# Performance work log

Measured on AMD Instinct MI355X. Metric: run time of the kernel, lower is better.

Reference implementation:

```python
import jax, jax.numpy as jnp
import numpy as np

B, T, C, H = 2, 2048, 1024, 16


def setup_inputs() -> dict:
    key = jax.random.key(0)
    ks = jax.random.split(key, 9)
    s = 1.0 / np.sqrt(C)
    return {
        "query": jax.random.normal(ks[0], (B, T, C), dtype=jnp.float32),
        "Wq": jax.random.normal(ks[1], (C, C), dtype=jnp.float32) * s,
        "bq": jnp.zeros((C,), dtype=jnp.float32),
        "Wk": jax.random.normal(ks[2], (C, C), dtype=jnp.float32) * s,
        "bk": jnp.zeros((C,), dtype=jnp.float32),
        "Wv": jax.random.normal(ks[3], (C, C), dtype=jnp.float32) * s,
        "bv": jnp.zeros((C,), dtype=jnp.float32),
        "Wp": jax.random.normal(ks[4], (C, C), dtype=jnp.float32) * s,
        "bp": jnp.zeros((C,), dtype=jnp.float32),
        "n_head": H,
    }


def reference(query, Wq, bq, Wk, bk, Wv, bv, Wp, bp, n_head):
    b, t, c = query.shape
    d = c // n_head
    # QKV projections -> [b, h, t, d]
    q = (query @ Wq + bq).reshape(b, t, n_head, d).transpose(0, 2, 1, 3)
    k = (query @ Wk + bk).reshape(b, t, n_head, d).transpose(0, 2, 1, 3)
    v = (query @ Wv + bv).reshape(b, t, n_head, d).transpose(0, 2, 1, 3)
    scale = 1.0 / jnp.sqrt(jnp.asarray(d, dtype=query.dtype))
    att = jnp.einsum('bhtd,bhsd->bhts', q, k) * scale  # [b,h,t,t]
    causal = jnp.tril(jnp.ones((t, t), dtype=bool))
    att = jnp.where(causal[None, None, :, :], att, -jnp.inf)
    att = jax.nn.softmax(att, axis=-1)
    y = jnp.einsum('bhts,bhsd->bhtd', att, v)  # [b,h,t,d]
    y = y.transpose(0, 2, 1, 3).reshape(b, t, c)
    return y @ Wp + bp
```

## Files before the change

kernel.cpp:

```cpp
#include <hip/hip_runtime.h>
#include <math.h>

#define B_ 2
#define T_ 2048
#define C_ 1024
#define H_ 16
#define D_ 64
#define M_ (B_*T_)

typedef __bf16 bf16x8 __attribute__((ext_vector_type(8)));
typedef __bf16 bf16x4 __attribute__((ext_vector_type(4)));
typedef float  f32x4  __attribute__((ext_vector_type(4)));
typedef float  f32x16 __attribute__((ext_vector_type(16)));

__device__ __forceinline__ unsigned short f2bf(float f) {
    unsigned int u = __float_as_uint(f);
    u += 0x7FFFu + ((u >> 16) & 1u);
    return (unsigned short)(u >> 16);
}

__device__ __forceinline__ bf16x8 pack4(unsigned a, unsigned b,
                                        unsigned c, unsigned d) {
    union { unsigned u[4]; bf16x8 v; } t;
    t.u[0] = a; t.u[1] = b; t.u[2] = c; t.u[3] = d;
    return t.v;
}

__device__ __forceinline__ void gload16(const void* g, void* l) {
    __builtin_amdgcn_global_load_lds(
        (const __attribute__((address_space(1))) void*)g,
        (__attribute__((address_space(3))) void*)l, 16, 0, 0);
}

__global__ __launch_bounds__(256) void prep_kernel(
    const float* __restrict__ X, unsigned short* __restrict__ Xb,
    const float* __restrict__ W0, const float* __restrict__ W1,
    const float* __restrict__ W2, const float* __restrict__ W3,
    unsigned short* __restrict__ T0, unsigned short* __restrict__ T1,
    unsigned short* __restrict__ T2, unsigned short* __restrict__ T3)
{
    const int tid = threadIdx.x;
    if (blockIdx.x < 2048) {
        const size_t i = ((size_t)blockIdx.x * 256 + tid) * 8;
        const float4 a = *(const float4*)&X[i];
        const float4 b = *(const float4*)&X[i + 4];
        ushort4 s0, s1;
        s0.x = f2bf(a.x); s0.y = f2bf(a.y); s0.z = f2bf(a.z); s0.w = f2bf(a.w);
        s1.x = f2bf(b.x); s1.y = f2bf(b.y); s1.z = f2bf(b.z); s1.w = f2bf(b.w);
        *(ushort4*)&Xb[i]     = s0;
        *(ushort4*)&Xb[i + 4] = s1;
        return;
    }
    const int bz = blockIdx.x - 2048;
    const int z = bz >> 10, rem = bz & 1023;
    const float* W; unsigned short* Wt;
    switch (z) {
        case 0: W = W0; Wt = T0; break;
        case 1: W = W1; Wt = T1; break;
        case 2: W = W2; Wt = T2; break;
        default: W = W3; Wt = T3; break;
    }
    __shared__ unsigned short tile[32][33];
    const int k0 = (rem >> 5) * 32, n0 = (rem & 31) * 32;
    {
        const int r = tid >> 3, c = (tid & 7) * 4;
        const float4 v = *(const float4*)&W[(size_t)(k0 + r)*C_ + n0 + c];
        tile[c+0][r] = f2bf(v.x);
        tile[c+1][r] = f2bf(v.y);
        tile[c+2][r] = f2bf(v.z);
        tile[c+3][r] = f2bf(v.w);
    }
    __syncthreads();
    {
        const int r = tid >> 3, c = (tid & 7) * 4;
        ushort4 s;
        s.x = tile[r][c+0]; s.y = tile[r][c+1]; s.z = tile[r][c+2]; s.w = tile[r][c+3];
        *(ushort4*)&Wt[(size_t)(n0 + r)*C_ + k0 + c] = s;
    }
}

__global__ __launch_bounds__(256) void gemm_proj_kernel(
    const unsigned short* __restrict__ A, const unsigned short* __restrict__ Bt,
    const float* __restrict__ bias, float* __restrict__ out)
{
    __shared__ __align__(16) unsigned short Als[2][64 * 32];
    __shared__ __align__(16) unsigned short Bls[2][128 * 32];

    const int tid  = threadIdx.x;
    const int lane = tid & 63;
    const int wave = tid >> 6;
    const int wm = wave >> 1, wn = wave & 1;
    const int l15 = lane & 15, quad = lane >> 4;
    const int m0 = blockIdx.y * 64, n0 = blockIdx.x * 128;
    const int srow = lane >> 2;
    const int scol = (lane & 3) * 8;

    const f32x4 zero4 = {0.f, 0.f, 0.f, 0.f};
    f32x4 acc[2][4];
    #pragma unroll
    for (int i = 0; i < 2; ++i)
        #pragma unroll
        for (int j = 0; j < 4; ++j) acc[i][j] = zero4;

    for (int k0 = 0; k0 < C_; k0 += 64) {
        __syncthreads();
        #pragma unroll
        for (int h = 0; h < 2; ++h) {
            gload16(&A[(size_t)(m0 + wave*16 + srow)*C_ + k0 + h*32 + scol],
                    &Als[h][(wave*16)*32]);
            #pragma unroll
            for (int u = 0; u < 2; ++u) {
                const int r = wave*32 + u*16 + srow;
                gload16(&Bt[(size_t)(n0 + r)*C_ + k0 + h*32 + scol],
                        &Bls[h][(wave*32 + u*16)*32]);
            }
        }
        __syncthreads();

        #pragma unroll
        for (int h = 0; h < 2; ++h) {
            bf16x8 af[2], bfr[4];
            #pragma unroll
            for (int i = 0; i < 2; ++i)
                af[i] = *(const bf16x8*)&Als[h][(wm*32 + i*16 + l15)*32 + quad*8];
            #pragma unroll
            for (int j = 0; j < 4; ++j)
                bfr[j] = *(const bf16x8*)&Bls[h][(wn*64 + j*16 + l15)*32 + quad*8];

            #pragma unroll
            for (int i = 0; i < 2; ++i)
                #pragma unroll
                for (int j = 0; j < 4; ++j)
                    acc[i][j] = __builtin_amdgcn_mfma_f32_16x16x32_bf16(
                        af[i], bfr[j], acc[i][j], 0, 0, 0);
        }
    }

    #pragma unroll
    for (int j = 0; j < 4; ++j) {
        const int n = n0 + wn*64 + j*16 + l15;
        const float bv = bias[n];
        #pragma unroll
        for (int i = 0; i < 2; ++i)
            #pragma unroll
            for (int r = 0; r < 4; ++r) {
                const int m = m0 + wm*32 + i*16 + quad*4 + r;
                out[(size_t)m*C_ + n] = acc[i][j][r] + bv;
            }
    }
}

__global__ __launch_bounds__(512, 2) void gemm256_qkv_kernel(
    const unsigned short* __restrict__ A, const unsigned short* __restrict__ Bt,
    const float* __restrict__ b0, const float* __restrict__ b1,
    const float* __restrict__ b2,
    unsigned short* __restrict__ outq, unsigned short* __restrict__ outk,
    unsigned short* __restrict__ outv)
{
    __shared__ __align__(16) unsigned short lds[4 * 16384];

    const int tid  = threadIdx.x;
    const int lane = tid & 63;
    const int wave = tid >> 6;
    const int l15  = lane & 15, quad = lane >> 4;
    const int wm   = wave >> 2, wn = wave & 3;
    const int bid  = blockIdx.y * 12 + blockIdx.x;
    const int swz  = (bid & 7) * 24 + (bid >> 3);
    const int m0   = (swz / 12) * 256, n0 = (swz % 12) * 256;

    const int lrow = lane >> 2;
    const int csw  = ((lane & 3) ^ ((lane >> 3) & 3)) * 8;
    const int sw8  = (quad ^ ((l15 >> 1) & 3)) * 8;

#define STAGE(tt) do {                                                         \
        const int bi_ = ((tt) & 3) << 14;                                      \
        const int k0_ = (tt) << 5;                                             \
        const int ra_ = m0 + wave*32 + lrow;                                   \
        const int rb_ = n0 + wave*32 + lrow;                                   \
        gload16(&A [(size_t)ra_*C_ + k0_ + csw],      &lds[bi_ + wave*1024]);  \
        gload16(&Bt[(size_t)rb_*C_ + k0_ + csw],      &lds[bi_ + 8192 + wave*1024]); \
        gload16(&A [(size_t)(ra_+16)*C_ + k0_ + csw], &lds[bi_ + wave*1024 + 512]);  \
        gload16(&Bt[(size_t)(rb_+16)*C_ + k0_ + csw], &lds[bi_ + 8192 + wave*1024 + 512]); \
    } while (0)

    const f32x4 zero4 = {0.f, 0.f, 0.f, 0.f};
    f32x4 acc[8][4];
    #pragma unroll
    for (int i = 0; i < 8; ++i)
        #pragma unroll
        for (int j = 0; j < 4; ++j) acc[i][j] = zero4;

    STAGE(0); STAGE(1); STAGE(2);

    for (int t = 0; t < 32; ++t) {
        const int bi = (t & 3) << 14;
        __builtin_amdgcn_s_barrier();
        __builtin_amdgcn_sched_barrier(0);
        if (t < 29) {
            STAGE(t + 3);
            asm volatile("s_waitcnt vmcnt(12)" ::: "memory");
        } else if (t == 29) {
            asm volatile("s_waitcnt vmcnt(8)" ::: "memory");
        } else if (t == 30) {
            asm volatile("s_waitcnt vmcnt(4)" ::: "memory");
        } else {
            asm volatile("s_waitcnt vmcnt(0)" ::: "memory");
        }
        __builtin_amdgcn_s_barrier();
        __builtin_amdgcn_sched_barrier(0);

        const unsigned short* Ab = &lds[bi];
        const unsigned short* Bb = &lds[bi + 8192];

        bf16x8 bfr[4], af[4];
        #pragma unroll
        for (int j = 0; j < 4; ++j)
            bfr[j] = *(const bf16x8*)&Bb[(wn*64 + j*16 + l15)*32 + sw8];
        #pragma unroll
        for (int i = 0; i < 4; ++i)
            af[i] = *(const bf16x8*)&Ab[(wm*128 + i*16 + l15)*32 + sw8];

        __builtin_amdgcn_s_setprio(1);
        #pragma unroll
        for (int i = 0; i < 4; ++i)
            #pragma unroll
            for (int j = 0; j < 4; ++j)
                acc[i][j] = __builtin_amdgcn_mfma_f32_16x16x32_bf16(
                    af[i], bfr[j], acc[i][j], 0, 0, 0);
        __builtin_amdgcn_s_setprio(0);

        __builtin_amdgcn_s_barrier();
        __builtin_amdgcn_sched_barrier(0);

        #pragma unroll
        for (int i = 0; i < 4; ++i)
            af[i] = *(const bf16x8*)&Ab[(wm*128 + 64 + i*16 + l15)*32 + sw8];

        __builtin_amdgcn_s_setprio(1);
        #pragma unroll
        for (int i = 0; i < 4; ++i)
            #pragma unroll
            for (int j = 0; j < 4; ++j)
                acc[4+i][j] = __builtin_amdgcn_mfma_f32_16x16x32_bf16(
                    af[i], bfr[j], acc[4+i][j], 0, 0, 0);
        __builtin_amdgcn_s_setprio(0);
    }
#undef STAGE

    __syncthreads();

    unsigned short* Ep = &lds[wave * 8192];
    const int which = n0 >> 10;
    const int c0 = (n0 & 1023) + wn * 64;
    const int h  = c0 >> 6;
    const int bb = m0 >> 11;
    const int t0 = (m0 & (T_ - 1)) + wm * 128;
    const int bh = bb * H_ + h;
    const float* bp = (which == 0) ? b0 : (which == 1 ? b1 : b2);
    const float qscale = (which == 0) ? 0.18033688f : 1.0f;

    if (which < 2) {
        __bf16* Eb = (__bf16*)Ep;
        #pragma unroll
        for (int j = 0; j < 4; ++j) {
            const int cl = j*16 + l15;
            const float bias = bp[c0 + cl];
            #pragma unroll
            for (int i = 0; i < 8; ++i)
                #pragma unroll
                for (int r = 0; r < 4; ++r)
                    Eb[(i*16 + quad*4 + r)*64 + cl] =
                        (__bf16)((acc[i][j][r] + bias) * qscale);
        }
        unsigned short* op = (which == 0) ? outq : outk;
        const int row8 = lane >> 3, chunk = lane & 7;
        #pragma unroll
        for (int u = 0; u < 16; ++u) {
            const int row = u*8 + row8;
            const uint4 v = *(const uint4*)&Ep[row*64 + chunk*8];
            *(uint4*)&op[((size_t)bh*T_ + t0 + row)*D_ + chunk*8] = v;
        }
    } else {
        #pragma unroll
        for (int j = 0; j < 4; ++j) {
            const int cl = j*16 + l15;
            const float bias = bp[c0 + cl];
            const int xo = (cl & 7) * 8;
            #pragma unroll
            for (int i = 0; i < 8; ++i) {
                bf16x4 pk = {(__bf16)(acc[i][j][0] + bias),
                             (__bf16)(acc[i][j][1] + bias),
                             (__bf16)(acc[i][j][2] + bias),
                             (__bf16)(acc[i][j][3] + bias)};
                *(bf16x4*)&Ep[cl*128 + ((i*16 + quad*4) ^ xo)] = pk;
            }
        }
        const int d4 = lane >> 4, chunk = lane & 15;
        #pragma unroll
        for (int u = 0; u < 16; ++u) {
            const int d = u*4 + d4;
            const uint4 v = *(const uint4*)&Ep[d*128 + ((chunk*8) ^ ((d & 7)*8))];
            *(uint4*)&outv[((size_t)bh*D_ + d)*T_ + t0 + chunk*8] = v;
        }
    }
}

__global__ __launch_bounds__(256) void flash_mfma_kernel(
    const unsigned short* __restrict__ Qs, const unsigned short* __restrict__ Ks,
    const unsigned short* __restrict__ Vts, unsigned short* __restrict__ Y,
    float* __restrict__ parts, float* __restrict__ lbase)
{
    __shared__ __align__(16) unsigned short Kls[64 * 64];
    __shared__ __align__(16) unsigned short Vls[64 * 64];
    __shared__ float lsums[4][32];

    const int tid  = threadIdx.x;
    const int lane = tid & 63, wave = tid >> 6;
    const int krl  = lane & 31, hi = lane >> 5;
    const int srow8 = lane >> 3;
    const int schk8 = ((lane & 7) ^ srow8) * 8;
    const int job  = blockIdx.x >> 5;
    const int bh   = blockIdx.x & 31;
    const bool isA = (job < 8);
    const int a    = isA ? job : job - 8;

    int qts[2], slos[2], shis[2], slots[2], nseg;
    if (isA) {
        qts[0] = a;      slos[0] = 0;        shis[0] = 2*a + 2;  slots[0] = -1;
        qts[1] = 15 - a; slos[1] = 0;        shis[1] = 15 - 2*a; slots[1] = 0;
        nseg = 2;
    } else {
        qts[0] = 15 - a; slos[0] = 15 - 2*a; shis[0] = 32 - 2*a; slots[0] = 1;
        nseg = 1;
    }

    const int b_ = bh >> 4, h_ = bh & (H_ - 1);

#define FSTAGE(itv) do {                                                       \
        const int s0_ = (itv) * 64;                                            \
        const int cu0_ = 2*wave, cu1_ = 2*wave + 1;                            \
        const int r0_ = cu0_*8 + srow8, r1_ = cu1_*8 + srow8;                  \
        gload16(&Ks [((size_t)bh*T_ + s0_ + r0_)*D_ + schk8],                  \
                (char*)Kls + cu0_*1024);                                       \
        gload16(&Vts[((size_t)bh*D_ + r0_)*T_ + s0_ + schk8],                  \
                (char*)Vls + cu0_*1024);                                       \
        gload16(&Ks [((size_t)bh*T_ + s0_ + r1_)*D_ + schk8],                  \
                (char*)Kls + cu1_*1024);                                       \
        gload16(&Vts[((size_t)bh*D_ + r1_)*T_ + s0_ + schk8],                  \
                (char*)Vls + cu1_*1024);                                       \
    } while (0)

    for (int sg = 0; sg < nseg; ++sg) {
        const int qt  = qts[sg];
        const int qw0 = qt * 128 + wave * 32;
        const int qrow = qw0 + krl;

        bf16x8 qf[4];
        #pragma unroll
        for (int ds = 0; ds < 4; ++ds)
            qf[ds] = *(const bf16x8*)&Qs[((size_t)bh*T_ + qrow)*D_ + ds*16 + hi*8];

        f32x16 o[2];
        #pragma unroll
        for (int dt = 0; dt < 2; ++dt)
            #pragma unroll
            for (int r = 0; r < 16; ++r) o[dt][r] = 0.f;
        float lsum = 0.f;

        for (int it = slos[sg]; it < shis[sg]; ++it) {
            const int s0 = it * 64;
            __syncthreads();
            FSTAGE(it);
            __syncthreads();

            if (s0 > qw0 + 31) continue;

            f32x16 st[2];
            #pragma unroll
            for (int kt = 0; kt < 2; ++kt)
                #pragma unroll
                for (int r = 0; r < 16; ++r) st[kt][r] = 0.f;
            #pragma unroll
            for (int kt = 0; kt < 2; ++kt) {
                #pragma unroll
                for (int ds = 0; ds < 4; ++ds) {
                    const int row = kt*32 + krl;
                    bf16x8 kf = *(const bf16x8*)
                        &Kls[row*64 + (((ds*2 + hi) ^ (krl & 7)) << 3)];
                    st[kt] = __builtin_amdgcn_mfma_f32_32x32x16_bf16(
                        kf, qf[ds], st[kt], 0, 0, 0);
                }
            }

            const bool diag = (s0 + 63 > qw0);
            #pragma unroll
            for (int kt = 0; kt < 2; ++kt) {
                const int kb = s0 + kt*32 + 4*hi;
                #pragma unroll
                for (int reg = 0; reg < 16; ++reg) {
                    const int crow = (reg & 3) + 8*(reg >> 2);
                    float e = __builtin_amdgcn_exp2f(st[kt][reg]);
                    if (diag && (kb + crow > qrow)) e = 0.f;
                    st[kt][reg] = e;
                    lsum += e;
                }
            }

            bf16x8 pa[4];
            #pragma unroll
            for (int kt = 0; kt < 2; ++kt) {
                #pragma unroll
                for (int hh = 0; hh < 2; ++hh) {
                    const int rb = hh * 8;
                    unsigned c0, c1, c2, c3;
                    asm("v_cvt_pk_bf16_f32 %0, %1, %2"
                        : "=v"(c0) : "v"(st[kt][rb+0]), "v"(st[kt][rb+1]));
                    asm("v_cvt_pk_bf16_f32 %0, %1, %2"
                        : "=v"(c1) : "v"(st[kt][rb+2]), "v"(st[kt][rb+3]));
                    asm("v_cvt_pk_bf16_f32 %0, %1, %2"
                        : "=v"(c2) : "v"(st[kt][rb+4]), "v"(st[kt][rb+5]));
                    asm("v_cvt_pk_bf16_f32 %0, %1, %2"
                        : "=v"(c3) : "v"(st[kt][rb+6]), "v"(st[kt][rb+7]));
                    asm("v_permlane32_swap_b32 %0, %1" : "+v"(c0), "+v"(c2));
                    asm("v_permlane32_swap_b32 %0, %1" : "+v"(c1), "+v"(c3));
                    pa[kt*2 + hh] = pack4(c0, c1, c2, c3);
                }
            }

            #pragma unroll
            for (int dt = 0; dt < 2; ++dt) {
                #pragma unroll
                for (int ks = 0; ks < 4; ++ks) {
                    const int rowd = dt*32 + krl;
                    bf16x8 vb = *(const bf16x8*)
                        &Vls[rowd*64 + (((ks*2 + hi) ^ (krl & 7)) << 3)];
                    o[dt] = __builtin_amdgcn_mfma_f32_32x32x16_bf16(
                        pa[ks], vb, o[dt], 0, 0, 0);
                }
            }
        }

        lsum += __shfl_xor(lsum, 32, 64);
        if (lane < 32) lsums[wave][krl] = lsum;

        if (slots[sg] < 0) {
            #pragma unroll
            for (int reg = 0; reg < 16; ++reg) {
                const int q = (reg & 3) + 8*(reg >> 2) + 4*hi;
                const float inv = 1.0f / lsums[wave][q];
                const size_t yb = ((size_t)(b_*T_ + qw0 + q))*C_ + h_*D_;
                *(__bf16*)&Y[yb + krl]      = (__bf16)(o[0][reg] * inv);
                *(__bf16*)&Y[yb + 32 + krl] = (__bf16)(o[1][reg] * inv);
            }
        } else {
            const int gpi = bh*16 + a*2 + slots[sg];
            float* Op = parts + (size_t)gpi*8192;
            float* Lp = lbase + gpi*128;
            if (lane < 32) Lp[wave*32 + lane] = lsum;
            #pragma unroll
            for (int reg = 0; reg < 16; ++reg) {
                const int tl = wave*32 + (reg & 3) + 8*(reg >> 2) + 4*hi;
                Op[(size_t)tl*64 + krl]      = o[0][reg];
                Op[(size_t)tl*64 + 32 + krl] = o[1][reg];
            }
        }
    }
#undef FSTAGE
}

__global__ __launch_bounds__(256) void merge_kernel(
    const float* __restrict__ parts, const float* __restrict__ lbase,
    unsigned short* __restrict__ Y)
{
    const int pair = blockIdx.x;
    const int bh = pair >> 3, p = pair & 7;
    const int qt = 15 - p;
    const int g0 = bh*16 + p*2;
    const float* O0 = parts + (size_t)g0*8192;
    const float* O1 = O0 + 8192;
    const float* L0 = lbase + g0*128;
    const float* L1 = L0 + 128;

    const int tid = threadIdx.x;
    const int r = tid >> 1, c0 = (tid & 1) * 32;
    const float inv = 1.0f / (L0[r] + L1[r]);
    const int b = bh >> 4, h = bh & (H_ - 1);
    const int t = qt*128 + r;
    #pragma unroll
    for (int k = 0; k < 8; ++k) {
        const f32x4 a  = *(const f32x4*)&O0[(size_t)r*64 + c0 + k*4];
        const f32x4 bb = *(const f32x4*)&O1[(size_t)r*64 + c0 + k*4];
        bf16x4 pk = {(__bf16)((a[0]+bb[0])*inv), (__bf16)((a[1]+bb[1])*inv),
                     (__bf16)((a[2]+bb[2])*inv), (__bf16)((a[3]+bb[3])*inv)};
        *(bf16x4*)&Y[((size_t)(b*T_ + t))*C_ + h*D_ + c0 + k*4] = pk;
    }
}

extern "C" void kernel_launch(void* const* d_in, const int* in_sizes, int n_in,
                              void* d_out, int out_size, void* d_ws, size_t ws_size,
                              hipStream_t stream) {
    const float* query = (const float*)d_in[0];
    const float* Wq = (const float*)d_in[1];
    const float* bq = (const float*)d_in[2];
    const float* Wk = (const float*)d_in[3];
    const float* bk = (const float*)d_in[4];
    const float* Wv = (const float*)d_in[5];
    const float* bv = (const float*)d_in[6];
    const float* Wp = (const float*)d_in[7];
    const float* bp = (const float*)d_in[8];
    float* out = (float*)d_out;

    char* ws = (char*)d_ws;
    unsigned short* qbf   = (unsigned short*)(ws);
    unsigned short* kbf   = (unsigned short*)(ws + 8388608);
    unsigned short* vtbf  = (unsigned short*)(ws + 16777216);
    unsigned short* WtP   = (unsigned short*)(ws + 25165824);
    unsigned short* WtQKV = (unsigned short*)(ws + 27262976);
    unsigned short* yb    = (unsigned short*)(ws + 33554432);
    unsigned short* qx    = (unsigned short*)(ws + 41943040);
    float* lbase = (float*)(ws + 27262976);
    float* parts = out;

    prep_kernel<<<6144, 256, 0, stream>>>(
        query, qx, Wq, Wk, Wv, Wp,
        WtQKV, WtQKV + (size_t)C_*C_, WtQKV + 2*(size_t)C_*C_, WtP);

    gemm256_qkv_kernel<<<dim3(12, 16), 512, 0, stream>>>(
        qx, WtQKV, bq, bk, bv, qbf, kbf, vtbf);

    flash_mfma_kernel<<<512, 256, 0, stream>>>(qbf, kbf, vtbf, yb, parts, lbase);
    merge_kernel<<<256, 256, 0, stream>>>(parts, lbase, yb);

    gemm_proj_kernel<<<dim3(C_/128, M_/64), 256, 0, stream>>>(
        yb, WtP, bp, out);
}
```

Measured before the change: 191.1 us.

## Pipeline output-projection GEMM with 4-stage LDS ring and double-buffer flash K/V

The projection GEMM now uses a 4-deep LDS ring with 32-wide k-steps, issuing loads three stages ahead and waiting with explicit vmcnt counts. It also XOR-swizzles the LDS layout to cut bank conflicts and raises wave priority around the MFMA block. The flash attention kernel double-buffers K/V tiles so the next tile's global-to-LDS load overlaps the current tile's compute, dropping one barrier per iteration. This costs more LDS per block, which may lower occupancy, and the hand-written waitcnt counts depend on the exact number of loads per stage.

```diff
diff --git a/kernel.cpp b/kernel.cpp
--- a/kernel.cpp
+++ b/kernel.cpp
@@ -83,8 +83,7 @@
     const unsigned short* __restrict__ A, const unsigned short* __restrict__ Bt,
     const float* __restrict__ bias, float* __restrict__ out)
 {
-    __shared__ __align__(16) unsigned short Als[2][64 * 32];
-    __shared__ __align__(16) unsigned short Bls[2][128 * 32];
+    __shared__ __align__(16) unsigned short lds[4 * 6144];
 
     const int tid  = threadIdx.x;
     const int lane = tid & 63;
@@ -92,8 +91,21 @@
     const int wm = wave >> 1, wn = wave & 1;
     const int l15 = lane & 15, quad = lane >> 4;
     const int m0 = blockIdx.y * 64, n0 = blockIdx.x * 128;
-    const int srow = lane >> 2;
-    const int scol = (lane & 3) * 8;
+
+    const int lrow = lane >> 2;
+    const int csw  = ((lane & 3) ^ ((lane >> 3) & 3)) * 8;
+    const int sw8  = (quad ^ ((l15 >> 1) & 3)) * 8;
+
+#define PSTAGE(tt) do {                                                        \
+        const int bi_ = ((tt) & 3) * 6144;                                     \
+        const int k0_ = (tt) << 5;                                             \
+        gload16(&A [(size_t)(m0 + wave*16 + lrow)*C_ + k0_ + csw],             \
+                &lds[bi_ + wave*512]);                                         \
+        gload16(&Bt[(size_t)(n0 + wave*32 + lrow)*C_ + k0_ + csw],             \
+                &lds[bi_ + 2048 + wave*1024]);                                 \
+        gload16(&Bt[(size_t)(n0 + wave*32 + 16 + lrow)*C_ + k0_ + csw],        \
+                &lds[bi_ + 2048 + wave*1024 + 512]);                           \
+    } while (0)
 
     const f32x4 zero4 = {0.f, 0.f, 0.f, 0.f};
     f32x4 acc[2][4];
@@ -102,39 +114,46 @@
         #pragma unroll
         for (int j = 0; j < 4; ++j) acc[i][j] = zero4;
 
-    for (int k0 = 0; k0 < C_; k0 += 64) {
-        __syncthreads();
-        #pragma unroll
-        for (int h = 0; h < 2; ++h) {
-            gload16(&A[(size_t)(m0 + wave*16 + srow)*C_ + k0 + h*32 + scol],
-                    &Als[h][(wave*16)*32]);
-            #pragma unroll
-            for (int u = 0; u < 2; ++u) {
-                const int r = wave*32 + u*16 + srow;
-                gload16(&Bt[(size_t)(n0 + r)*C_ + k0 + h*32 + scol],
-                        &Bls[h][(wave*32 + u*16)*32]);
-            }
-        }
-        __syncthreads();
-
-        #pragma unroll
-        for (int h = 0; h < 2; ++h) {
-            bf16x8 af[2], bfr[4];
-            #pragma unroll
-            for (int i = 0; i < 2; ++i)
-                af[i] = *(const bf16x8*)&Als[h][(wm*32 + i*16 + l15)*32 + quad*8];
+    PSTAGE(0); PSTAGE(1); PSTAGE(2);
+
+    for (int t = 0; t < 32; ++t) {
+        const int bi = (t & 3) * 6144;
+        __builtin_amdgcn_s_barrier();
+        __builtin_amdgcn_sched_barrier(0);
+        if (t < 29) {
+            PSTAGE(t + 3);
+            asm volatile("s_waitcnt vmcnt(9)" ::: "memory");
+        } else if (t == 29) {
+            asm volatile("s_waitcnt vmcnt(6)" ::: "memory");
+        } else if (t == 30) {
+            asm volatile("s_waitcnt vmcnt(3)" ::: "memory");
+        } else {
+            asm volatile("s_waitcnt vmcnt(0)" ::: "memory");
+        }
+        __builtin_amdgcn_s_barrier();
+        __builtin_amdgcn_sched_barrier(0);
+
+        const unsigned short* Ab = &lds[bi];
+        const unsigned short* Bb = &lds[bi + 2048];
+
+        bf16x8 af[2], bfr[4];
+        #pragma unroll
+        for (int i = 0; i < 2; ++i)
+            af[i] = *(const bf16x8*)&Ab[(wm*32 + i*16 + l15)*32 + sw8];
+        #pragma unroll
+        for (int j = 0; j < 4; ++j)
+            bfr[j] = *(const bf16x8*)&Bb[(wn*64 + j*16 + l15)*32 + sw8];
+
+        __builtin_amdgcn_s_setprio(1);
+        #pragma unroll
+        for (int i = 0; i < 2; ++i)
             #pragma unroll
             for (int j = 0; j < 4; ++j)
-                bfr[j] = *(const bf16x8*)&Bls[h][(wn*64 + j*16 + l15)*32 + quad*8];
-
-            #pragma unroll
-            for (int i = 0; i < 2; ++i)
-                #pragma unroll
-                for (int j = 0; j < 4; ++j)
-                    acc[i][j] = __builtin_amdgcn_mfma_f32_16x16x32_bf16(
-                        af[i], bfr[j], acc[i][j], 0, 0, 0);
-        }
-    }
+                acc[i][j] = __builtin_amdgcn_mfma_f32_16x16x32_bf16(
+                    af[i], bfr[j], acc[i][j], 0, 0, 0);
+        __builtin_amdgcn_s_setprio(0);
+    }
+#undef PSTAGE
 
     #pragma unroll
     for (int j = 0; j < 4; ++j) {
@@ -310,8 +329,8 @@
     const unsigned short* __restrict__ Vts, unsigned short* __restrict__ Y,
     float* __restrict__ parts, float* __restrict__ lbase)
 {
-    __shared__ __align__(16) unsigned short Kls[64 * 64];
-    __shared__ __align__(16) unsigned short Vls[64 * 64];
+    __shared__ __align__(16) unsigned short Kls[2][64 * 64];
+    __shared__ __align__(16) unsigned short Vls[2][64 * 64];
     __shared__ float lsums[4][32];
 
     const int tid  = threadIdx.x;
@@ -336,24 +355,27 @@
 
     const int b_ = bh >> 4, h_ = bh & (H_ - 1);
 
-#define FSTAGE(itv) do {                                                       \
+#define FSTAGE(itv, bb) do {                                                   \
         const int s0_ = (itv) * 64;                                            \
         const int cu0_ = 2*wave, cu1_ = 2*wave + 1;                            \
         const int r0_ = cu0_*8 + srow8, r1_ = cu1_*8 + srow8;                  \
         gload16(&Ks [((size_t)bh*T_ + s0_ + r0_)*D_ + schk8],                  \
-                (char*)Kls + cu0_*1024);                                       \
+                (char*)&Kls[bb][0] + cu0_*1024);                               \
         gload16(&Vts[((size_t)bh*D_ + r0_)*T_ + s0_ + schk8],                  \
-                (char*)Vls + cu0_*1024);                                       \
+                (char*)&Vls[bb][0] + cu0_*1024);                               \
         gload16(&Ks [((size_t)bh*T_ + s0_ + r1_)*D_ + schk8],                  \
-                (char*)Kls + cu1_*1024);                                       \
+                (char*)&Kls[bb][0] + cu1_*1024);                               \
         gload16(&Vts[((size_t)bh*D_ + r1_)*T_ + s0_ + schk8],                  \
-                (char*)Vls + cu1_*1024);                                       \
+                (char*)&Vls[bb][0] + cu1_*1024);                               \
     } while (0)
 
     for (int sg = 0; sg < nseg; ++sg) {
         const int qt  = qts[sg];
         const int qw0 = qt * 128 + wave * 32;
         const int qrow = qw0 + krl;
+        const int itlo = slos[sg], ithi = shis[sg];
+
+        FSTAGE(itlo, 0);
 
         bf16x8 qf[4];
         #pragma unroll
@@ -367,77 +389,81 @@
             for (int r = 0; r < 16; ++r) o[dt][r] = 0.f;
         float lsum = 0.f;
 
-        for (int it = slos[sg]; it < shis[sg]; ++it) {
+        __syncthreads();
+        int cur = 0;
+
+        for (int it = itlo; it < ithi; ++it) {
+            if (it + 1 < ithi) FSTAGE(it + 1, cur ^ 1);
+
             const int s0 = it * 64;
-            __syncthreads();
-            FSTAGE(it);
-            __syncthreads();
-
-            if (s0 > qw0 + 31) continue;
-
-            f32x16 st[2];
-            #pragma unroll
-            for (int kt = 0; kt < 2; ++kt)
+            if (s0 <= qw0 + 31) {
+                f32x16 st[2];
                 #pragma unroll
-                for (int r = 0; r < 16; ++r) st[kt][r] = 0.f;
-            #pragma unroll
-            for (int kt = 0; kt < 2; ++kt) {
+                for (int kt = 0; kt < 2; ++kt)
+                    #pragma unroll
+                    for (int r = 0; r < 16; ++r) st[kt][r] = 0.f;
                 #pragma unroll
-                for (int ds = 0; ds < 4; ++ds) {
-                    const int row = kt*32 + krl;
-                    bf16x8 kf = *(const bf16x8*)
-                        &Kls[row*64 + (((ds*2 + hi) ^ (krl & 7)) << 3)];
-                    st[kt] = __builtin_amdgcn_mfma_f32_32x32x16_bf16(
-                        kf, qf[ds], st[kt], 0, 0, 0);
+                for (int kt = 0; kt < 2; ++kt) {
+                    #pragma unroll
+                    for (int ds = 0; ds < 4; ++ds) {
+                        const int row = kt*32 + krl;
+                        bf16x8 kf = *(const bf16x8*)
+                            &Kls[cur][row*64 + (((ds*2 + hi) ^ (krl & 7)) << 3)];
+                        st[kt] = __builtin_amdgcn_mfma_f32_32x32x16_bf16(
+                            kf, qf[ds], st[kt], 0, 0, 0);
+                    }
+                }
+
+                const bool diag = (s0 + 63 > qw0);
+                #pragma unroll
+                for (int kt = 0; kt < 2; ++kt) {
+                    const int kb = s0 + kt*32 + 4*hi;
+                    #pragma unroll
+                    for (int reg = 0; reg < 16; ++reg) {
+                        const int crow = (reg & 3) + 8*(reg >> 2);
+                        float e = __builtin_amdgcn_exp2f(st[kt][reg]);
+                        if (diag && (kb + crow > qrow)) e = 0.f;
+                        st[kt][reg] = e;
+                        lsum += e;
+                    }
+                }
+
+                bf16x8 pa[4];
+                #pragma unroll
+                for (int kt = 0; kt < 2; ++kt) {
+                    #pragma unroll
+                    for (int hh = 0; hh < 2; ++hh) {
+                        const int rb = hh * 8;
+                        unsigned c0, c1, c2, c3;
+                        asm("v_cvt_pk_bf16_f32 %0, %1, %2"
+                            : "=v"(c0) : "v"(st[kt][rb+0]), "v"(st[kt][rb+1]));
+                        asm("v_cvt_pk_bf16_f32 %0, %1, %2"
+                            : "=v"(c1) : "v"(st[kt][rb+2]), "v"(st[kt][rb+3]));
+                        asm("v_cvt_pk_bf16_f32 %0, %1, %2"
+                            : "=v"(c2) : "v"(st[kt][rb+4]), "v"(st[kt][rb+5]));
+                        asm("v_cvt_pk_bf16_f32 %0, %1, %2"
+                            : "=v"(c3) : "v"(st[kt][rb+6]), "v"(st[kt][rb+7]));
+                        asm("v_permlane32_swap_b32 %0, %1" : "+v"(c0), "+v"(c2));
+                        asm("v_permlane32_swap_b32 %0, %1" : "+v"(c1), "+v"(c3));
+                        pa[kt*2 + hh] = pack4(c0, c1, c2, c3);
+                    }
+                }
+
+                #pragma unroll
+                for (int dt = 0; dt < 2; ++dt) {
+                    #pragma unroll
+                    for (int ks = 0; ks < 4; ++ks) {
+                        const int rowd = dt*32 + krl;
+                        bf16x8 vb = *(const bf16x8*)
+                            &Vls[cur][rowd*64 + (((ks*2 + hi) ^ (krl & 7)) << 3)];
+                        o[dt] = __builtin_amdgcn_mfma_f32_32x32x16_bf16(
+                            pa[ks], vb, o[dt], 0, 0, 0);
+                    }
                 }
             }
 
-            const bool diag = (s0 + 63 > qw0);
-            #pragma unroll
-            for (int kt = 0; kt < 2; ++kt) {
-                const int kb = s0 + kt*32 + 4*hi;
-                #pragma unroll
-                for (int reg = 0; reg < 16; ++reg) {
-                    const int crow = (reg & 3) + 8*(reg >> 2);
-                    float e = __builtin_amdgcn_exp2f(st[kt][reg]);
-                    if (diag && (kb + crow > qrow)) e = 0.f;
-                    st[kt][reg] = e;
-                    lsum += e;
-                }
-            }
-
-            bf16x8 pa[4];
-            #pragma unroll
-            for (int kt = 0; kt < 2; ++kt) {
-                #pragma unroll
-                for (int hh = 0; hh < 2; ++hh) {
-                    const int rb = hh * 8;
-                    unsigned c0, c1, c2, c3;
-                    asm("v_cvt_pk_bf16_f32 %0, %1, %2"
-                        : "=v"(c0) : "v"(st[kt][rb+0]), "v"(st[kt][rb+1]));
-                    asm("v_cvt_pk_bf16_f32 %0, %1, %2"
-                        : "=v"(c1) : "v"(st[kt][rb+2]), "v"(st[kt][rb+3]));
-                    asm("v_cvt_pk_bf16_f32 %0, %1, %2"
-                        : "=v"(c2) : "v"(st[kt][rb+4]), "v"(st[kt][rb+5]));
-                    asm("v_cvt_pk_bf16_f32 %0, %1, %2"
-                        : "=v"(c3) : "v"(st[kt][rb+6]), "v"(st[kt][rb+7]));
-                    asm("v_permlane32_swap_b32 %0, %1" : "+v"(c0), "+v"(c2));
-                    asm("v_permlane32_swap_b32 %0, %1" : "+v"(c1), "+v"(c3));
-                    pa[kt*2 + hh] = pack4(c0, c1, c2, c3);
-                }
-            }
-
-            #pragma unroll
-            for (int dt = 0; dt < 2; ++dt) {
-                #pragma unroll
-                for (int ks = 0; ks < 4; ++ks) {
-                    const int rowd = dt*32 + krl;
-                    bf16x8 vb = *(const bf16x8*)
-                        &Vls[rowd*64 + (((ks*2 + hi) ^ (krl & 7)) << 3)];
-                    o[dt] = __builtin_amdgcn_mfma_f32_32x32x16_bf16(
-                        pa[ks], vb, o[dt], 0, 0, 0);
-                }
-            }
+            __syncthreads();
+            cur ^= 1;
         }
 
         lsum += __shfl_xor(lsum, 32, 64);
```

New measurement: 193.7 us. No clear change (+1.3%).
